# Kernel tuning notes

Hardware: AMD Instinct MI355X
Metric: run time of the kernel (lower is better)

## Reference

```python
import jax, jax.numpy as jnp
import numpy as np

D = 512
B = 8
N = 4096  # h = w = 64 grid


def _rmsnorm(x, eps=1e-6):
    # SimpleRMSNorm (no learned scale)
    return x * jax.lax.rsqrt(jnp.mean(jnp.square(x), axis=-1, keepdims=True) + eps)


def setup_inputs() -> dict:
    key = jax.random.key(0)
    ks = jax.random.split(key, 8)
    s = 1.0 / np.sqrt(D)
    return {
        "x": jax.random.normal(ks[0], (B, N, D), jnp.float32),
        "lower_bound": jax.random.uniform(ks[1], (1,), jnp.float32),
        "W_in": jax.random.normal(ks[2], (D, D), jnp.float32) * s,
        "b_in": jnp.zeros((D,), jnp.float32),
        "W_f": jax.random.normal(ks[3], (D, D), jnp.float32) * s,
        "b_f": jnp.zeros((D,), jnp.float32),
        "theta": jax.random.normal(ks[4], (D,), jnp.float32),
        "W_g": jax.random.normal(ks[5], (D, D), jnp.float32) * s,
        "b_g": jnp.zeros((D,), jnp.float32),
        "W_out": jax.random.normal(ks[6], (D, D), jnp.float32) * s,
        "b_out": jnp.zeros((D,), jnp.float32),
    }


def _gated_scan(decay, u, axis, reverse):
    # linear recurrence h_t = decay_t * h_{t-1} + u_t via associative scan
    def comb(e1, e2):
        a1, x1 = e1
        a2, x2 = e2
        return a1 * a2, a2 * x1 + x2
    _, y = jax.lax.associative_scan(comb, (decay, u), axis=axis, reverse=reverse)
    return y


def reference(x, lower_bound, W_in, b_in, W_f, b_f, theta, W_g, b_g, W_out, b_out):
    b, n, d = x.shape
    h = int(np.sqrt(n))
    w = n // h
    # b n d -> n b d -> h w b d
    xg = jnp.transpose(x, (1, 0, 2)).reshape(h, w, b, d)
    u = jax.nn.silu(xg @ W_in + b_in)              # candidate input
    f = jax.nn.sigmoid(xg @ W_f + b_f)             # forget gate
    lam = lower_bound + (1.0 - lower_bound) * f    # lower-bounded decay magnitude
    # complex decay lam * exp(i theta); complex input (1 - lam) * u
    decay = (lam * jnp.cos(theta) + 1j * (lam * jnp.sin(theta))).astype(jnp.complex64)
    inp = ((1.0 - lam) * u).astype(jnp.complex64)
    # bidirectional 2D scan: forward/backward over both grid axes (non-causal)
    hidden = jnp.zeros_like(u)
    for axis in (0, 1):
        for rev in (False, True):
            hidden = hidden + _gated_scan(decay, inp, axis, rev).real
    g = jax.nn.sigmoid(xg @ W_g + b_g)             # output gate
    y = (g * _rmsnorm(hidden)) @ W_out + b_out
    # h w b d -> n b d -> b n d
    return jnp.transpose(y.reshape(n, b, d), (1, 0, 2))
```

## Files before the change

### kernel.cpp

```cpp
#include <hip/hip_runtime.h>
#include <math.h>

#define DD 512
#define HG 64
#define M_ROWS 32768
#define ELEMS ((size_t)M_ROWS * DD)
#define LOG2E 1.44269504088896340736f

typedef __attribute__((ext_vector_type(8))) _Float16 f16x8;
typedef __attribute__((ext_vector_type(2))) _Float16 f16x2;
typedef __attribute__((ext_vector_type(4))) float f32x4;

__device__ __forceinline__ float fexp2_(float x) { return __builtin_amdgcn_exp2f(x); }
__device__ __forceinline__ float frcp_(float x)  { return __builtin_amdgcn_rcpf(x); }
__device__ __forceinline__ float fsig_(float v)  { return frcp_(1.0f + fexp2_(-v * LOG2E)); }

__global__ __launch_bounds__(256) void prep(
    const float* __restrict__ x, _Float16* __restrict__ x16,
    const float* __restrict__ W0, const float* __restrict__ W1,
    const float* __restrict__ W2, const float* __restrict__ W3,
    _Float16* __restrict__ WT)
{
    __shared__ float tile[64][65];
    if (blockIdx.x < 8192) {
        const size_t i = ((size_t)blockIdx.x * 256 + threadIdx.x) * 8;
        const float4 a = *(const float4*)&x[i];
        const float4 b = *(const float4*)&x[i + 4];
        f16x8 h;
        h[0] = (_Float16)a.x; h[1] = (_Float16)a.y;
        h[2] = (_Float16)a.z; h[3] = (_Float16)a.w;
        h[4] = (_Float16)b.x; h[5] = (_Float16)b.y;
        h[6] = (_Float16)b.z; h[7] = (_Float16)b.w;
        *(f16x8*)&x16[i] = h;
        return;
    }
    const int wb = blockIdx.x - 8192;
    const int z = wb >> 6;
    const int rem = wb & 63;
    const int n0 = (rem & 7) * 64, k0 = (rem >> 3) * 64;
    const float* W = (z == 0) ? W0 : (z == 1) ? W1 : (z == 2) ? W2 : W3;
    _Float16* dst = WT + (size_t)z * DD * DD;
    const int t = threadIdx.x;
    const int tr = t >> 6, tc = t & 63;
#pragma unroll
    for (int p = 0; p < 16; ++p)
        tile[p * 4 + tr][tc] = W[(size_t)(k0 + p * 4 + tr) * DD + n0 + tc];
    __syncthreads();
#pragma unroll
    for (int p = 0; p < 16; ++p) {
        const int nn = p * 4 + tr;
        dst[(size_t)(n0 + nn) * DD + k0 + tc] = (_Float16)tile[tc][nn];
    }
}

template <int MODE>
__global__ __launch_bounds__(512, 2) void gemm8p(
    const _Float16* __restrict__ A, const _Float16* __restrict__ WT,
    const float* __restrict__ b0, const float* __restrict__ b1,
    const float* __restrict__ b2, const float* __restrict__ lb_ptr,
    void* __restrict__ o0, void* __restrict__ o1, void* __restrict__ o2)
{
    __shared__ __align__(16) _Float16 As[2][256][64];
    __shared__ __align__(16) _Float16 Bs[2][256][64];

    const int NB = (MODE == 0) ? 6 : 2;
    const int lin = blockIdx.x;
    const int xcd = lin & 7;
    const int qq  = lin >> 3;
    const int n_idx = qq % NB;
    const int mq  = qq / NB;
    const int m0 = (xcd + 8 * mq) * 256;
    const int n0 = n_idx * 256;

    const int tid  = threadIdx.x;
    const int wv   = tid >> 6;
    const int lane = tid & 63;
    const int wm = wv >> 2, wn = wv & 3;
    const int lrow = lane & 15;
    const int lk   = lane >> 4;

    const int srow8 = wv * 8 + (lane >> 3);
    const int sswz  = ((lane & 7) ^ (lane >> 3)) * 8;

    const _Float16* Ag = A  + (size_t)m0 * DD;
    const _Float16* Bg = WT + (size_t)n0 * DD;

    f32x4 acc[8][4];
#pragma unroll
    for (int i = 0; i < 8; ++i)
#pragma unroll
        for (int j = 0; j < 4; ++j) acc[i][j] = (f32x4)(0.f);

#define STG(LDSBUF, GPTR, P_, HALF_, KT_) do {                                 \
    _Pragma("unroll")                                                          \
    for (int j_ = 0; j_ < 2; ++j_) {                                           \
        __builtin_amdgcn_global_load_lds(                                      \
            (const __attribute__((address_space(1))) void*)                    \
              (GPTR + (size_t)((HALF_)*128 + j_*64 + srow8) * DD               \
                     + (KT_)*64 + sswz),                                       \
            (__attribute__((address_space(3))) void*)                          \
              &LDSBUF[P_][(HALF_)*128 + j_*64 + wv*8][0], 16, 0, 0);           \
    } } while (0)

#define LDA(P_, HA_) do {                                                      \
    _Pragma("unroll")                                                          \
    for (int q_ = 0; q_ < 4; ++q_)                                             \
    _Pragma("unroll")                                                          \
    for (int ks_ = 0; ks_ < 2; ++ks_)                                          \
        aA[q_][ks_] = *(const f16x8*)((const char*)&As[P_][0][0]               \
            + (size_t)((wm*64 + q_*16 + (HA_)*128 + lrow) * 128                \
            + (((ks_*4 + lk) ^ (lrow & 7)) * 16)));                            \
    } while (0)

#define LDB(DST_, P_, HB_) do {                                                \
    _Pragma("unroll")                                                          \
    for (int q_ = 0; q_ < 2; ++q_)                                             \
    _Pragma("unroll")                                                          \
    for (int ks_ = 0; ks_ < 2; ++ks_)                                          \
        DST_[q_][ks_] = *(const f16x8*)((const char*)&Bs[P_][0][0]             \
            + (size_t)((wn*32 + q_*16 + (HB_)*128 + lrow) * 128                \
            + (((ks_*4 + lk) ^ (lrow & 7)) * 16)));                            \
    } while (0)

#define MMQ(HA_, BSET_, BOFF_) do {                                            \
    __builtin_amdgcn_s_setprio(1);                                             \
    _Pragma("unroll")                                                          \
    for (int q_ = 0; q_ < 4; ++q_)                                             \
    _Pragma("unroll")                                                          \
    for (int n_ = 0; n_ < 2; ++n_)                                             \
    _Pragma("unroll")                                                          \
    for (int ks_ = 0; ks_ < 2; ++ks_)                                          \
        acc[(HA_)*4 + q_][(BOFF_) + n_] =                                      \
            __builtin_amdgcn_mfma_f32_16x16x32_f16(                            \
                aA[q_][ks_], BSET_[n_][ks_], acc[(HA_)*4 + q_][(BOFF_) + n_],  \
                0, 0, 0);                                                      \
    __builtin_amdgcn_s_setprio(0);                                             \
    } while (0)

#define BAR __builtin_amdgcn_s_barrier()
#define VM(N_) asm volatile("s_waitcnt vmcnt(" #N_ ")" ::: "memory")

    f16x8 aA[4][2], bB0[2][2], bB1[2][2];

    STG(As, Ag, 0, 0, 0);
    STG(Bs, Bg, 0, 0, 0);
    STG(Bs, Bg, 0, 1, 0);
    STG(As, Ag, 0, 1, 0);
    STG(As, Ag, 1, 0, 1);
    STG(Bs, Bg, 1, 0, 1);
    STG(Bs, Bg, 1, 1, 1);
    VM(10); BAR;

    for (int g = 0; g < 6; ++g) {
        const int p = g & 1;
        LDA(p, 0); LDB(bB0, p, 0);
        STG(As, Ag, p ^ 1, 1, g + 1);
        BAR;
        MMQ(0, bB0, 0);
        VM(10); BAR;
        LDB(bB1, p, 1);
        STG(As, Ag, p, 0, g + 2);
        BAR;
        MMQ(0, bB1, 2);
        VM(10); BAR;
        LDA(p, 1);
        STG(Bs, Bg, p, 0, g + 2);
        BAR;
        MMQ(1, bB1, 2);
        BAR;
        STG(Bs, Bg, p, 1, g + 2);
        BAR;
        MMQ(1, bB0, 0);
        VM(10); BAR;
    }

    LDA(0, 0); LDB(bB0, 0, 0);
    STG(As, Ag, 1, 1, 7);
    BAR; MMQ(0, bB0, 0); VM(10); BAR;
    LDB(bB1, 0, 1);
    BAR; MMQ(0, bB1, 2); VM(8); BAR;
    LDA(0, 1);
    BAR; MMQ(1, bB1, 2); BAR;
    MMQ(1, bB0, 0);
    VM(4); BAR;

    LDA(1, 0); LDB(bB0, 1, 0);
    BAR; MMQ(0, bB0, 0); VM(2); BAR;
    LDB(bB1, 1, 1);
    BAR; MMQ(0, bB1, 2); VM(0); BAR;
    LDA(1, 1);
    BAR; MMQ(1, bB1, 2); BAR;
    MMQ(1, bB0, 0);

#undef STG
#undef LDA
#undef LDB
#undef MMQ
#undef BAR
#undef VM

    if (MODE == 0) {
        const int seg = n_idx >> 1;
        const float lbv = lb_ptr[0];
        const float* bias = (seg == 0) ? b0 : (seg == 1) ? b1 : b2;
        _Float16* outp = (seg == 0) ? (_Float16*)o0
                       : (seg == 1) ? (_Float16*)o1 : (_Float16*)o2;
        const int cbase = (n_idx & 1) * 256 + wn * 32;
#pragma unroll
        for (int a = 0; a < 8; ++a) {
            const int row = m0 + wm * 64 + (a & 3) * 16 + (a >> 2) * 128 + lk * 4;
#pragma unroll
            for (int b = 0; b < 4; ++b) {
                const int col = cbase + (b & 1) * 16 + (b >> 1) * 128 + lrow;
                const float bcol = bias[col];
#pragma unroll
                for (int r = 0; r < 4; ++r) {
                    const float v = acc[a][b][r] + bcol;
                    float res;
                    if (seg == 0)      res = (1.0f - lbv) * frcp_(1.0f + fexp2_(v * LOG2E));
                    else if (seg == 1) res = v * fsig_(v);
                    else               res = fsig_(v);
                    outp[(size_t)(row + r) * DD + col] = (_Float16)res;
                }
            }
        }
    } else {
        float* outp = (float*)o0;
#pragma unroll
        for (int a = 0; a < 8; ++a) {
            const int row = m0 + wm * 64 + (a & 3) * 16 + (a >> 2) * 128 + lk * 4;
#pragma unroll
            for (int b = 0; b < 4; ++b) {
                const int col = n0 + wn * 32 + (b & 1) * 16 + (b >> 1) * 128 + lrow;
                const float bcol = b0[col];
#pragma unroll
                for (int r = 0; r < 4; ++r)
                    outp[(size_t)(row + r) * DD + col] = acc[a][b][r] + bcol;
            }
        }
    }
}

#define CH 4
#define CL 16

#define STEP(K, YR0, YI0, YR1, YI1) {                                      \
    const float dm0_ = (float)dmr[K][0], dm1_ = (float)dmr[K][1];          \
    const float lm0_ = 1.0f - dm0_, lm1_ = 1.0f - dm1_;                    \
    float nr_ = fmaf(lm0_, c0 * (YR0) - s0 * (YI0), dm0_ * (float)ur[K][0]); \
    YI0 = lm0_ * (c0 * (YI0) + s0 * (YR0)); YR0 = nr_;                     \
    nr_ = fmaf(lm1_, c1 * (YR1) - s1 * (YI1), dm1_ * (float)ur[K][1]);     \
    YI1 = lm1_ * (c1 * (YI1) + s1 * (YR1)); YR1 = nr_; }

__global__ __launch_bounds__(256, 4) void scan2(
    const _Float16* __restrict__ dm, const _Float16* __restrict__ u,
    const float* __restrict__ theta,
    _Float16* __restrict__ ha, _Float16* __restrict__ hb)
{
    __shared__ float ex[CH][64][13];

    const int blk  = blockIdx.x & 2047;
    const bool is_i = blockIdx.x >= 2048;
    const int tid   = threadIdx.x;
    const int chunk = tid >> 6;
    const int dpl   = tid & 63;
    const int dpg   = blk & 3;
    const int line  = blk >> 2;
    const int d0    = (dpg * 64 + dpl) * 2;

    size_t base, stride;
    _Float16* hout;
    if (!is_i) {
        base = (size_t)line * (HG * DD) + d0; stride = DD; hout = ha;
    } else {
        const int bb = line >> 6, j = line & 63;
        base = (size_t)bb * (HG * HG * DD) + (size_t)j * DD + d0;
        stride = (size_t)HG * DD; hout = hb;
    }
    const size_t cbase = base + (size_t)(chunk * CL) * stride;

    float s0, c0, s1, c1;
    sincosf(theta[d0], &s0, &c0);
    sincosf(theta[d0 + 1], &s1, &c1);

    f16x2 dmr[CL], ur[CL];
#pragma unroll
    for (int k = 0; k < CL; ++k) {
        dmr[k] = *(const f16x2*)&dm[cbase + (size_t)k * stride];
        ur[k]  = *(const f16x2*)&u [cbase + (size_t)k * stride];
    }

    float fr0 = 0.f, fi0 = 0.f, fr1 = 0.f, fi1 = 0.f;
    float P0 = 1.f, P1 = 1.f;
#pragma unroll
    for (int k = 0; k < CL; ++k) {
        const float dm0_ = (float)dmr[k][0], dm1_ = (float)dmr[k][1];
        const float lm0_ = 1.0f - dm0_, lm1_ = 1.0f - dm1_;
        P0 *= lm0_; P1 *= lm1_;
        float nr_ = fmaf(lm0_, c0 * fr0 - s0 * fi0, dm0_ * (float)ur[k][0]);
        fi0 = lm0_ * (c0 * fi0 + s0 * fr0); fr0 = nr_;
        nr_ = fmaf(lm1_, c1 * fr1 - s1 * fi1, dm1_ * (float)ur[k][1]);
        fi1 = lm1_ * (c1 * fi1 + s1 * fr1); fr1 = nr_;
    }
    float br0 = 0.f, bi0 = 0.f, br1 = 0.f, bi1 = 0.f;
#pragma unroll
    for (int k = CL - 1; k >= 0; --k) STEP(k, br0, bi0, br1, bi1);

    float rc0 = c0, rs0 = s0, rc1 = c1, rs1 = s1;
#pragma unroll
    for (int q = 0; q < 4; ++q) {
        float t0 = rc0 * rc0 - rs0 * rs0; rs0 = 2.f * rc0 * rs0; rc0 = t0;
        float t1 = rc1 * rc1 - rs1 * rs1; rs1 = 2.f * rc1 * rs1; rc1 = t1;
    }

    {
        float* e = ex[chunk][dpl];
        e[0]  = P0 * rc0; e[1]  = P0 * rs0;
        e[2]  = fr0;      e[3]  = fi0;
        e[4]  = br0;      e[5]  = bi0;
        e[6]  = P1 * rc1; e[7]  = P1 * rs1;
        e[8]  = fr1;      e[9]  = fi1;
        e[10] = br1;      e[11] = bi1;
    }
    __syncthreads();

    float cfr0 = 0.f, cfi0 = 0.f, cfr1 = 0.f, cfi1 = 0.f;
    for (int cc = 0; cc < chunk; ++cc) {
        const float* e = ex[cc][dpl];
        float nr = e[2] + e[0] * cfr0 - e[1] * cfi0;
        cfi0     = e[3] + e[0] * cfi0 + e[1] * cfr0;
        cfr0 = nr;
        nr       = e[8] + e[6] * cfr1 - e[7] * cfi1;
        cfi1     = e[9] + e[6] * cfi1 + e[7] * cfr1;
        cfr1 = nr;
    }
    float cbr0 = 0.f, cbi0 = 0.f, cbr1 = 0.f, cbi1 = 0.f;
    for (int cc = CH - 1; cc > chunk; --cc) {
        const float* e = ex[cc][dpl];
        float nr = e[4] + e[0] * cbr0 - e[1] * cbi0;
        cbi0     = e[5] + e[0] * cbi0 + e[1] * cbr0;
        cbr0 = nr;
        nr       = e[10] + e[6] * cbr1 - e[7] * cbi1;
        cbi1     = e[11] + e[6] * cbi1 + e[7] * cbr1;
        cbr1 = nr;
    }

    float yr0 = cfr0, yi0 = cfi0, yr1 = cfr1, yi1 = cfi1;
    f16x2 fres[CL];
#pragma unroll
    for (int k = 0; k < CL; ++k) {
        STEP(k, yr0, yi0, yr1, yi1);
        f16x2 p; p[0] = (_Float16)yr0; p[1] = (_Float16)yr1;
        fres[k] = p;
    }
    yr0 = cbr0; yi0 = cbi0; yr1 = cbr1; yi1 = cbi1;
#pragma unroll
    for (int k = CL - 1; k >= 0; --k) {
        STEP(k, yr0, yi0, yr1, yi1);
        f16x2 o;
        o[0] = (_Float16)((float)fres[k][0] + yr0);
        o[1] = (_Float16)((float)fres[k][1] + yr1);
        *(f16x2*)&hout[cbase + (size_t)k * stride] = o;
    }
}
#undef STEP

__global__ __launch_bounds__(256) void gate_rmsnorm(
    const _Float16* __restrict__ ha, const _Float16* __restrict__ hb,
    const _Float16* __restrict__ g, _Float16* __restrict__ v)
{
    const int row = blockIdx.x;
    const int t = threadIdx.x;
    const size_t b0 = (size_t)row * DD + t * 2;
    const f16x2 a = *(const f16x2*)&ha[b0];
    const f16x2 b = *(const f16x2*)&hb[b0];
    const float h0 = (float)a[0] + (float)b[0];
    const float h1 = (float)a[1] + (float)b[1];
    float ss = h0 * h0 + h1 * h1;
#pragma unroll
    for (int off = 32; off > 0; off >>= 1) ss += __shfl_down(ss, off, 64);
    __shared__ float wsum[4];
    __shared__ float rms_s;
    if ((t & 63) == 0) wsum[t >> 6] = ss;
    __syncthreads();
    if (t == 0) {
        const float tot = wsum[0] + wsum[1] + wsum[2] + wsum[3];
        rms_s = rsqrtf(tot * (1.0f / (float)DD) + 1e-6f);
    }
    __syncthreads();
    const float rms = rms_s;
    const f16x2 gg = *(const f16x2*)&g[b0];
    f16x2 o;
    o[0] = (_Float16)((float)gg[0] * h0 * rms);
    o[1] = (_Float16)((float)gg[1] * h1 * rms);
    *(f16x2*)&v[b0] = o;
}

extern "C" void kernel_launch(void* const* d_in, const int* in_sizes, int n_in,
                              void* d_out, int out_size, void* d_ws, size_t ws_size,
                              hipStream_t stream)
{
    const float* x     = (const float*)d_in[0];
    const float* lb    = (const float*)d_in[1];
    const float* W_in  = (const float*)d_in[2];
    const float* b_in  = (const float*)d_in[3];
    const float* W_f   = (const float*)d_in[4];
    const float* b_f   = (const float*)d_in[5];
    const float* theta = (const float*)d_in[6];
    const float* W_g   = (const float*)d_in[7];
    const float* b_g   = (const float*)d_in[8];
    const float* W_out = (const float*)d_in[9];
    const float* b_out = (const float*)d_in[10];

    float* out = (float*)d_out;
    char* wsb  = (char*)d_ws;

    _Float16* dm_v = (_Float16*)wsb;
    _Float16* u_b  = (_Float16*)(wsb + ELEMS * 2);
    _Float16* g_b  = (_Float16*)(wsb + ELEMS * 4);
    _Float16* WT   = (_Float16*)(wsb + ELEMS * 6);
    const size_t WSEG = (size_t)DD * DD;

    _Float16* ha  = (_Float16*)d_out;
    _Float16* x16 = (_Float16*)((char*)d_out + ELEMS * 2);
    _Float16* hb  = x16;

    prep<<<8448, 256, 0, stream>>>(x, x16, W_f, W_in, W_g, W_out, WT);

    gemm8p<0><<<768, 512, 0, stream>>>(x16, WT, b_f, b_in, b_g, lb,
                                       dm_v, u_b, g_b);

    scan2<<<4096, 256, 0, stream>>>(dm_v, u_b, theta, ha, hb);

    gate_rmsnorm<<<M_ROWS, 256, 0, stream>>>(ha, hb, g_b, dm_v);

    gemm8p<1><<<256, 512, 0, stream>>>(dm_v, WT + 3 * WSEG, b_out, nullptr,
                                       nullptr, nullptr, out, nullptr, nullptr);
}
```

Baseline: 283.0 us.

## Restructure GEMM mainloop into 4-stage k32 pipeline with register double-buffering

Replaces the 2-buffer k64 LDS schedule, split into halves with many barriers, with a 4-deep ring of k32 LDS stages. Each iteration issues one global-to-LDS prefetch three stages ahead, loads the next stage's fragments into alternate registers and runs 32 MFMAs, with one barrier per step. The warp tile also changes from split 64+64 rows and 32+32 columns to contiguous 128x64 blocks. The aim is to cut barrier count and improve load/compute overlap. The XOR swizzle is dropped, so LDS reads of 128-byte rows may now hit bank conflicts, and double-buffered fragments raise register pressure.

```diff
diff --git a/kernel.cpp b/kernel.cpp
--- a/kernel.cpp
+++ b/kernel.cpp
@@ -60,8 +60,8 @@
     const float* __restrict__ b2, const float* __restrict__ lb_ptr,
     void* __restrict__ o0, void* __restrict__ o1, void* __restrict__ o2)
 {
-    __shared__ __align__(16) _Float16 As[2][256][64];
-    __shared__ __align__(16) _Float16 Bs[2][256][64];
+    __shared__ __align__(16) _Float16 As[4][256][32];
+    __shared__ __align__(16) _Float16 Bs[4][256][32];
 
     const int NB = (MODE == 0) ? 6 : 2;
     const int lin = blockIdx.x;
@@ -79,11 +79,10 @@
     const int lrow = lane & 15;
     const int lk   = lane >> 4;
 
-    const int srow8 = wv * 8 + (lane >> 3);
-    const int sswz  = ((lane & 7) ^ (lane >> 3)) * 8;
-
-    const _Float16* Ag = A  + (size_t)m0 * DD;
-    const _Float16* Bg = WT + (size_t)n0 * DD;
+    const int srow = wv * 32 + (lane >> 2);
+    const int schk = (lane & 3) * 8;
+    const _Float16* Ag = A  + (size_t)(m0 + srow) * DD + schk;
+    const _Float16* Bg = WT + (size_t)(n0 + srow) * DD + schk;
 
     f32x4 acc[8][4];
 #pragma unroll
@@ -91,111 +90,66 @@
 #pragma unroll
         for (int j = 0; j < 4; ++j) acc[i][j] = (f32x4)(0.f);
 
-#define STG(LDSBUF, GPTR, P_, HALF_, KT_) do {                                 \
+#define STG(BUF_, KT_) do {                                                    \
     _Pragma("unroll")                                                          \
     for (int j_ = 0; j_ < 2; ++j_) {                                           \
         __builtin_amdgcn_global_load_lds(                                      \
             (const __attribute__((address_space(1))) void*)                    \
-              (GPTR + (size_t)((HALF_)*128 + j_*64 + srow8) * DD               \
-                     + (KT_)*64 + sswz),                                       \
+              (Ag + (size_t)(j_ * 16) * DD + (KT_) * 32),                      \
             (__attribute__((address_space(3))) void*)                          \
-              &LDSBUF[P_][(HALF_)*128 + j_*64 + wv*8][0], 16, 0, 0);           \
+              &As[BUF_][wv * 32 + j_ * 16][0], 16, 0, 0);                      \
+        __builtin_amdgcn_global_load_lds(                                      \
+            (const __attribute__((address_space(1))) void*)                    \
+              (Bg + (size_t)(j_ * 16) * DD + (KT_) * 32),                      \
+            (__attribute__((address_space(3))) void*)                          \
+              &Bs[BUF_][wv * 32 + j_ * 16][0], 16, 0, 0);                      \
     } } while (0)
 
-#define LDA(P_, HA_) do {                                                      \
-    _Pragma("unroll")                                                          \
-    for (int q_ = 0; q_ < 4; ++q_)                                             \
-    _Pragma("unroll")                                                          \
-    for (int ks_ = 0; ks_ < 2; ++ks_)                                          \
-        aA[q_][ks_] = *(const f16x8*)((const char*)&As[P_][0][0]               \
-            + (size_t)((wm*64 + q_*16 + (HA_)*128 + lrow) * 128                \
-            + (((ks_*4 + lk) ^ (lrow & 7)) * 16)));                            \
+#define LDF(FA_, FB_, BUF_) do {                                               \
+    _Pragma("unroll")                                                          \
+    for (int q_ = 0; q_ < 8; ++q_)                                             \
+        FA_[q_] = *(const f16x8*)&As[BUF_][wm * 128 + q_ * 16 + lrow][lk * 8]; \
+    _Pragma("unroll")                                                          \
+    for (int n_ = 0; n_ < 4; ++n_)                                             \
+        FB_[n_] = *(const f16x8*)&Bs[BUF_][wn * 64 + n_ * 16 + lrow][lk * 8];  \
     } while (0)
 
-#define LDB(DST_, P_, HB_) do {                                                \
-    _Pragma("unroll")                                                          \
-    for (int q_ = 0; q_ < 2; ++q_)                                             \
-    _Pragma("unroll")                                                          \
-    for (int ks_ = 0; ks_ < 2; ++ks_)                                          \
-        DST_[q_][ks_] = *(const f16x8*)((const char*)&Bs[P_][0][0]             \
-            + (size_t)((wn*32 + q_*16 + (HB_)*128 + lrow) * 128                \
-            + (((ks_*4 + lk) ^ (lrow & 7)) * 16)));                            \
-    } while (0)
-
-#define MMQ(HA_, BSET_, BOFF_) do {                                            \
+#define MM(FA_, FB_) do {                                                      \
     __builtin_amdgcn_s_setprio(1);                                             \
     _Pragma("unroll")                                                          \
-    for (int q_ = 0; q_ < 4; ++q_)                                             \
-    _Pragma("unroll")                                                          \
-    for (int n_ = 0; n_ < 2; ++n_)                                             \
-    _Pragma("unroll")                                                          \
-    for (int ks_ = 0; ks_ < 2; ++ks_)                                          \
-        acc[(HA_)*4 + q_][(BOFF_) + n_] =                                      \
-            __builtin_amdgcn_mfma_f32_16x16x32_f16(                            \
-                aA[q_][ks_], BSET_[n_][ks_], acc[(HA_)*4 + q_][(BOFF_) + n_],  \
-                0, 0, 0);                                                      \
+    for (int q_ = 0; q_ < 8; ++q_)                                             \
+    _Pragma("unroll")                                                          \
+    for (int n_ = 0; n_ < 4; ++n_)                                             \
+        acc[q_][n_] = __builtin_amdgcn_mfma_f32_16x16x32_f16(                  \
+            FA_[q_], FB_[n_], acc[q_][n_], 0, 0, 0);                           \
     __builtin_amdgcn_s_setprio(0);                                             \
     } while (0)
 
 #define BAR __builtin_amdgcn_s_barrier()
 #define VM(N_) asm volatile("s_waitcnt vmcnt(" #N_ ")" ::: "memory")
 
-    f16x8 aA[4][2], bB0[2][2], bB1[2][2];
-
-    STG(As, Ag, 0, 0, 0);
-    STG(Bs, Bg, 0, 0, 0);
-    STG(Bs, Bg, 0, 1, 0);
-    STG(As, Ag, 0, 1, 0);
-    STG(As, Ag, 1, 0, 1);
-    STG(Bs, Bg, 1, 0, 1);
-    STG(Bs, Bg, 1, 1, 1);
-    VM(10); BAR;
-
-    for (int g = 0; g < 6; ++g) {
-        const int p = g & 1;
-        LDA(p, 0); LDB(bB0, p, 0);
-        STG(As, Ag, p ^ 1, 1, g + 1);
-        BAR;
-        MMQ(0, bB0, 0);
-        VM(10); BAR;
-        LDB(bB1, p, 1);
-        STG(As, Ag, p, 0, g + 2);
-        BAR;
-        MMQ(0, bB1, 2);
-        VM(10); BAR;
-        LDA(p, 1);
-        STG(Bs, Bg, p, 0, g + 2);
-        BAR;
-        MMQ(1, bB1, 2);
-        BAR;
-        STG(Bs, Bg, p, 1, g + 2);
-        BAR;
-        MMQ(1, bB0, 0);
-        VM(10); BAR;
-    }
-
-    LDA(0, 0); LDB(bB0, 0, 0);
-    STG(As, Ag, 1, 1, 7);
-    BAR; MMQ(0, bB0, 0); VM(10); BAR;
-    LDB(bB1, 0, 1);
-    BAR; MMQ(0, bB1, 2); VM(8); BAR;
-    LDA(0, 1);
-    BAR; MMQ(1, bB1, 2); BAR;
-    MMQ(1, bB0, 0);
+    f16x8 FA0[8], FB0[4], FA1[8], FB1[4];
+
+    STG(0, 0); STG(1, 1); STG(2, 2);
     VM(4); BAR;
-
-    LDA(1, 0); LDB(bB0, 1, 0);
-    BAR; MMQ(0, bB0, 0); VM(2); BAR;
-    LDB(bB1, 1, 1);
-    BAR; MMQ(0, bB1, 2); VM(0); BAR;
-    LDA(1, 1);
-    BAR; MMQ(1, bB1, 2); BAR;
-    MMQ(1, bB0, 0);
+    LDF(FA0, FB0, 0);
+
+#pragma unroll
+    for (int g = 0; g < 16; ++g) {
+        if (g + 3 < 16) STG((g + 3) & 3, g + 3);
+        if (g + 1 < 16) {
+            if (g & 1) LDF(FA0, FB0, (g + 1) & 3);
+            else       LDF(FA1, FB1, (g + 1) & 3);
+        }
+        if (g & 1) MM(FA1, FB1);
+        else       MM(FA0, FB0);
+        if (g < 13)      { VM(4); BAR; }
+        else if (g < 15) { VM(0); BAR; }
+    }
 
 #undef STG
-#undef LDA
-#undef LDB
-#undef MMQ
+#undef LDF
+#undef MM
 #undef BAR
 #undef VM
 
@@ -205,17 +159,17 @@
         const float* bias = (seg == 0) ? b0 : (seg == 1) ? b1 : b2;
         _Float16* outp = (seg == 0) ? (_Float16*)o0
                        : (seg == 1) ? (_Float16*)o1 : (_Float16*)o2;
-        const int cbase = (n_idx & 1) * 256 + wn * 32;
-#pragma unroll
-        for (int a = 0; a < 8; ++a) {
-            const int row = m0 + wm * 64 + (a & 3) * 16 + (a >> 2) * 128 + lk * 4;
-#pragma unroll
-            for (int b = 0; b < 4; ++b) {
-                const int col = cbase + (b & 1) * 16 + (b >> 1) * 128 + lrow;
+        const int cbase = (n_idx & 1) * 256 + wn * 64;
+#pragma unroll
+        for (int q = 0; q < 8; ++q) {
+            const int row = m0 + wm * 128 + q * 16 + lk * 4;
+#pragma unroll
+            for (int n = 0; n < 4; ++n) {
+                const int col = cbase + n * 16 + lrow;
                 const float bcol = bias[col];
 #pragma unroll
                 for (int r = 0; r < 4; ++r) {
-                    const float v = acc[a][b][r] + bcol;
+                    const float v = acc[q][n][r] + bcol;
                     float res;
                     if (seg == 0)      res = (1.0f - lbv) * frcp_(1.0f + fexp2_(v * LOG2E));
                     else if (seg == 1) res = v * fsig_(v);
@@ -227,15 +181,15 @@
     } else {
         float* outp = (float*)o0;
 #pragma unroll
-        for (int a = 0; a < 8; ++a) {
-            const int row = m0 + wm * 64 + (a & 3) * 16 + (a >> 2) * 128 + lk * 4;
-#pragma unroll
-            for (int b = 0; b < 4; ++b) {
-                const int col = n0 + wn * 32 + (b & 1) * 16 + (b >> 1) * 128 + lrow;
+        for (int q = 0; q < 8; ++q) {
+            const int row = m0 + wm * 128 + q * 16 + lk * 4;
+#pragma unroll
+            for (int n = 0; n < 4; ++n) {
+                const int col = n0 + wn * 64 + n * 16 + lrow;
                 const float bcol = b0[col];
 #pragma unroll
                 for (int r = 0; r < 4; ++r)
-                    outp[(size_t)(row + r) * DD + col] = acc[a][b][r] + bcol;
+                    outp[(size_t)(row + r) * DD + col] = acc[q][n][r] + bcol;
             }
         }
     }
```

After: 287.1 us. Within noise of the previous version (+1.4%).
